# Optimization experiments

Measured on AMD Instinct MI355X. Metric: run time of the kernel, lower is better.

The kernel has to match this reference:

```python
import jax, jax.numpy as jnp
import numpy as np

B, S, D = 2, 2048, 1024
E = 4
H = 4 * D  # MLP hidden; SwiGLU w_v outputs 2*H


def setup_inputs() -> dict:
    key = jax.random.key(0)
    k_x, k_r, k_wv, k_wp = jax.random.split(key, 4)
    x = jax.random.normal(k_x, (B, S, D), dtype=jnp.float32)
    w_router = jax.random.normal(k_r, (D, E), dtype=jnp.float32) * 0.02
    # stacked expert weights, stored [in, out] (transpose of torch Linear)
    w_v = jax.random.normal(k_wv, (E, D, 2 * H), dtype=jnp.float32) * 0.02
    w_proj = jax.random.normal(k_wp, (E, H, D), dtype=jnp.float32) * 0.02
    return {"x": x, "w_router": w_router, "w_v": w_v, "w_proj": w_proj}


def reference(x, w_router, w_v, w_proj):
    # router: softmax then argmax (top-1); output NOT scaled by prob (matches torch src)
    logits = jnp.einsum("bsd,de->bse", x, w_router)
    probs = jax.nn.softmax(logits, axis=-1)
    expert_idx = jnp.argmax(probs, axis=-1)  # [B,S]
    # dense per-expert SwiGLU MLP: gv [E,B,S,2H]
    gv = jnp.einsum("bsd,edh->ebsh", x, w_v)
    gate_raw, value = jnp.split(gv, 2, axis=-1)
    h = gate_raw * jax.nn.sigmoid(gate_raw) * value  # beta=1.0 SiLU gate
    y = jnp.einsum("ebsh,ehd->ebsd", h, w_proj)  # [E,B,S,D]
    onehot = jax.nn.one_hot(expert_idx, w_v.shape[0], dtype=x.dtype)  # [B,S,E]
    return jnp.einsum("bse,ebsd->bsd", onehot, y)
```

## Files before the change

kernel.cpp:

```cpp
#include <hip/hip_runtime.h>


#define TTOK 4096
#define DIN  1024
#define HDIM 4096
#define H2   8192
#define TPAD 4608

typedef float f32x4 __attribute__((ext_vector_type(4)));
typedef __bf16 bf16x8 __attribute__((ext_vector_type(8)));
typedef unsigned short u16x8 __attribute__((ext_vector_type(8)));
typedef unsigned short u16x4 __attribute__((ext_vector_type(4)));

__device__ __forceinline__ unsigned short f2b(float f) {
  unsigned int u = __builtin_bit_cast(unsigned int, f);
  u += 0x7fffu + ((u >> 16) & 1u);
  return (unsigned short)(u >> 16);
}

__device__ __forceinline__ void gload16(const void* g, void* l) {
  __builtin_amdgcn_global_load_lds(
      (const __attribute__((address_space(1))) unsigned int*)g,
      (__attribute__((address_space(3))) unsigned int*)l, 16, 0, 0);
}

__global__ __launch_bounds__(256) void k_router(const float* __restrict__ x,
    const float* __restrict__ wrt, int* __restrict__ eidx,
    int* __restrict__ rank, int* __restrict__ cnt) {
  const int w = threadIdx.x >> 6, lane = threadIdx.x & 63;
  const int t = blockIdx.x * 4 + w;
  const float* xr = x + (size_t)t * DIN;
  const float4* w4 = (const float4*)wrt;
  float a0 = 0.f, a1 = 0.f, a2 = 0.f, a3 = 0.f;
  for (int k = 0; k < DIN; k += 64) {
    float xv = xr[k + lane];
    float4 ww = w4[k + lane];
    a0 += xv * ww.x; a1 += xv * ww.y; a2 += xv * ww.z; a3 += xv * ww.w;
  }
  #pragma unroll
  for (int off = 32; off; off >>= 1) {
    a0 += __shfl_xor(a0, off); a1 += __shfl_xor(a1, off);
    a2 += __shfl_xor(a2, off); a3 += __shfl_xor(a3, off);
  }
  if (lane == 0) {
    int e = 0; float b = a0;
    if (a1 > b) { b = a1; e = 1; }
    if (a2 > b) { b = a2; e = 2; }
    if (a3 > b) { b = a3; e = 3; }
    eidx[t] = e;
    rank[t] = atomicAdd(&cnt[e], 1);
  }
}

__global__ void k_setup(const int* __restrict__ cnt, int* __restrict__ poff,
                        int* __restrict__ tExp, int* __restrict__ tRow,
                        int* __restrict__ nMt) {
  int p = 0, nm = 0;
  for (int e = 0; e < 4; e++) {
    poff[e] = p;
    int mt = (cnt[e] + 127) >> 7;
    for (int i = 0; i < mt; i++) { tExp[nm] = e; tRow[nm] = p + i * 128; nm++; }
    p += mt * 128;
  }
  poff[4] = p;
  *nMt = nm;
}

__global__ __launch_bounds__(256) void k_scatter(const int* __restrict__ eidx,
    const int* __restrict__ rank, const int* __restrict__ poff,
    int* __restrict__ perm) {
  const int t = blockIdx.x * 256 + threadIdx.x;
  const int pos = poff[eidx[t]] + rank[t];
  perm[pos] = t;
}

__global__ __launch_bounds__(256) void k_gather(const float* __restrict__ x,
    const int* __restrict__ perm, unsigned short* __restrict__ A) {
  const int r = blockIdx.x;
  const int t = perm[r];
  unsigned short* dst = A + (size_t)r * DIN + threadIdx.x * 4;
  if (t < 0) {
    u16x4 z{0, 0, 0, 0};
    *(u16x4*)dst = z;
  } else {
    float4 v = *(const float4*)(x + (size_t)t * DIN + threadIdx.x * 4);
    u16x4 o{f2b(v.x), f2b(v.y), f2b(v.z), f2b(v.w)};
    *(u16x4*)dst = o;
  }
}

__global__ __launch_bounds__(256) void k_transpose(const float* __restrict__ src,
    unsigned short* __restrict__ dst, int K, int N) {
  __shared__ __align__(16) unsigned short T[64][72];
  const int n0 = blockIdx.x * 64, k0 = blockIdx.y * 64;
  const size_t eoff = (size_t)blockIdx.z * K * N;
  const int tid = threadIdx.x;
  const int rr = tid >> 4;
  const int cc = (tid & 15) * 4;
  #pragma unroll
  for (int i = 0; i < 4; i++) {
    const int r = rr + i * 16;
    float4 v = *(const float4*)(src + eoff + (size_t)(k0 + r) * N + n0 + cc);
    T[cc + 0][r] = f2b(v.x);
    T[cc + 1][r] = f2b(v.y);
    T[cc + 2][r] = f2b(v.z);
    T[cc + 3][r] = f2b(v.w);
  }
  __syncthreads();
  const int n = tid >> 2, kc = (tid & 3) * 16;
  u16x8 a = *(const u16x8*)&T[n][kc];
  u16x8 b = *(const u16x8*)&T[n][kc + 8];
  unsigned short* dp = dst + eoff + (size_t)(n0 + n) * K + k0 + kc;
  *(u16x8*)(dp) = a;
  *(u16x8*)(dp + 8) = b;
}

__global__ __launch_bounds__(256) void k_gemm1(const unsigned short* __restrict__ A,
    const unsigned short* __restrict__ Wt, unsigned short* __restrict__ Hb,
    const int* __restrict__ tExp, const int* __restrict__ tRow,
    const int* __restrict__ nMt) {
  if ((int)blockIdx.y >= *nMt) return;
  __shared__ __align__(16) unsigned short As[128 * 32];
  __shared__ __align__(16) unsigned short Bg[128 * 32];
  __shared__ __align__(16) unsigned short Bv[128 * 32];
  const int e = tExp[blockIdx.y];
  const int row0 = tRow[blockIdx.y];
  const int n0 = blockIdx.x * 128;
  const int tid = threadIdx.x, lane = tid & 63;
  const int w = tid >> 6, wr = w >> 1, wc = w & 1;
  const int rl = lane >> 2;
  const int kc = (lane & 3) * 8;
  const int mrow = lane & 15, krow = (lane >> 4) * 8;

  const unsigned short* aG  = A  + (size_t)(row0 + w * 16 + rl) * DIN + kc;
  const unsigned short* bgG = Wt + (size_t)e * H2 * DIN
                                 + (size_t)(n0 + w * 16 + rl) * DIN + kc;
  const unsigned short* bvG = bgG + (size_t)HDIM * DIN;

  f32x4 accg[4][4], accv[4][4];
  #pragma unroll
  for (int i = 0; i < 4; i++)
    #pragma unroll
    for (int j = 0; j < 4; j++) {
      accg[i][j] = f32x4{0.f, 0.f, 0.f, 0.f};
      accv[i][j] = f32x4{0.f, 0.f, 0.f, 0.f};
    }

  for (int k0 = 0; k0 < DIN; k0 += 32) {
    gload16(aG + k0,                     &As[w * 512]);
    gload16(aG + k0 + (size_t)64 * DIN,  &As[w * 512 + 2048]);
    gload16(bgG + k0,                    &Bg[w * 512]);
    gload16(bgG + k0 + (size_t)64 * DIN, &Bg[w * 512 + 2048]);
    gload16(bvG + k0,                    &Bv[w * 512]);
    gload16(bvG + k0 + (size_t)64 * DIN, &Bv[w * 512 + 2048]);
    __syncthreads();
    u16x8 af[4], bg[4], bv[4];
    #pragma unroll
    for (int f = 0; f < 4; f++) {
      af[f] = *(const u16x8*)&As[(wr * 64 + f * 16 + mrow) * 32 + krow];
      bg[f] = *(const u16x8*)&Bg[(wc * 64 + f * 16 + mrow) * 32 + krow];
      bv[f] = *(const u16x8*)&Bv[(wc * 64 + f * 16 + mrow) * 32 + krow];
    }
    #pragma unroll
    for (int fn = 0; fn < 4; fn++)
      #pragma unroll
      for (int fm = 0; fm < 4; fm++) {
        accg[fm][fn] = __builtin_amdgcn_mfma_f32_16x16x32_bf16(
            __builtin_bit_cast(bf16x8, af[fm]), __builtin_bit_cast(bf16x8, bg[fn]),
            accg[fm][fn], 0, 0, 0);
        accv[fm][fn] = __builtin_amdgcn_mfma_f32_16x16x32_bf16(
            __builtin_bit_cast(bf16x8, af[fm]), __builtin_bit_cast(bf16x8, bv[fn]),
            accv[fm][fn], 0, 0, 0);
      }
    __syncthreads();
  }
  #pragma unroll
  for (int fm = 0; fm < 4; fm++) {
    const int rbase = row0 + wr * 64 + fm * 16 + (lane >> 4) * 4;
    #pragma unroll
    for (int fn = 0; fn < 4; fn++) {
      const int col = n0 + wc * 64 + fn * 16 + mrow;
      #pragma unroll
      for (int j = 0; j < 4; j++) {
        float g = accg[fm][fn][j];
        float v = accv[fm][fn][j];
        float h = g / (1.f + __expf(-g)) * v;
        Hb[(size_t)(rbase + j) * HDIM + col] = f2b(h);
      }
    }
  }
}

__global__ __launch_bounds__(256) void k_gemm2(const unsigned short* __restrict__ Hb,
    const unsigned short* __restrict__ Wt, float* __restrict__ out,
    const int* __restrict__ tExp, const int* __restrict__ tRow,
    const int* __restrict__ nMt, const int* __restrict__ perm) {
  const int my = blockIdx.y >> 1;
  const int ks = blockIdx.y & 1;
  if (my >= *nMt) return;
  __shared__ __align__(16) unsigned short As[128 * 32];
  __shared__ __align__(16) unsigned short Bs[128 * 32];
  const int e = tExp[my];
  const int row0 = tRow[my];
  const int n0 = blockIdx.x * 128;
  const int tid = threadIdx.x, lane = tid & 63;
  const int w = tid >> 6, wr = w >> 1, wc = w & 1;
  const int rl = lane >> 2, kc = (lane & 3) * 8;
  const int mrow = lane & 15, krow = (lane >> 4) * 8;

  const unsigned short* aG = Hb + (size_t)(row0 + w * 16 + rl) * HDIM + ks * 2048 + kc;
  const unsigned short* bG = Wt + (size_t)e * DIN * HDIM
                                + (size_t)(n0 + w * 16 + rl) * HDIM + ks * 2048 + kc;
  f32x4 acc[4][4];
  #pragma unroll
  for (int i = 0; i < 4; i++)
    #pragma unroll
    for (int j = 0; j < 4; j++) acc[i][j] = f32x4{0.f, 0.f, 0.f, 0.f};

  for (int k0 = 0; k0 < 2048; k0 += 32) {
    gload16(aG + k0,                      &As[w * 512]);
    gload16(aG + k0 + (size_t)64 * HDIM,  &As[w * 512 + 2048]);
    gload16(bG + k0,                      &Bs[w * 512]);
    gload16(bG + k0 + (size_t)64 * HDIM,  &Bs[w * 512 + 2048]);
    __syncthreads();
    u16x8 af[4], bf[4];
    #pragma unroll
    for (int f = 0; f < 4; f++) {
      af[f] = *(const u16x8*)&As[(wr * 64 + f * 16 + mrow) * 32 + krow];
      bf[f] = *(const u16x8*)&Bs[(wc * 64 + f * 16 + mrow) * 32 + krow];
    }
    #pragma unroll
    for (int fn = 0; fn < 4; fn++)
      #pragma unroll
      for (int fm = 0; fm < 4; fm++)
        acc[fm][fn] = __builtin_amdgcn_mfma_f32_16x16x32_bf16(
            __builtin_bit_cast(bf16x8, af[fm]), __builtin_bit_cast(bf16x8, bf[fn]),
            acc[fm][fn], 0, 0, 0);
    __syncthreads();
  }
  #pragma unroll
  for (int fm = 0; fm < 4; fm++) {
    const int rbase = row0 + wr * 64 + fm * 16 + (lane >> 4) * 4;
    #pragma unroll
    for (int fn = 0; fn < 4; fn++) {
      const int col = n0 + wc * 64 + fn * 16 + mrow;
      #pragma unroll
      for (int j = 0; j < 4; j++) {
        const int t = perm[rbase + j];
        if (t >= 0) atomicAdd(&out[(size_t)t * DIN + col], acc[fm][fn][j]);
      }
    }
  }
}

extern "C" void kernel_launch(void* const* d_in, const int* in_sizes, int n_in,
                              void* d_out, int out_size, void* d_ws, size_t ws_size,
                              hipStream_t stream) {
  const float* x        = (const float*)d_in[0];
  const float* w_router = (const float*)d_in[1];
  const float* w_v      = (const float*)d_in[2];
  const float* w_proj   = (const float*)d_in[3];
  float* out = (float*)d_out;
  char* ws = (char*)d_ws;

  int* cnt  = (int*)(ws + 0);
  int* nMt  = (int*)(ws + 16);
  int* poff = (int*)(ws + 32);
  int* tExp = (int*)(ws + 128);
  int* tRow = (int*)(ws + 320);
  int* eidx = (int*)(ws + 512);
  int* rank = (int*)(ws + 512 + 16384);
  int* perm = (int*)(ws + 512 + 32768);
  unsigned short* Abuf = (unsigned short*)(ws + 52224);
  unsigned short* Hbuf = (unsigned short*)(ws + 9489408);
  unsigned short* Wvt  = (unsigned short*)(ws + 47238144);
  unsigned short* Wpt  = (unsigned short*)(ws + 114347008);

  hipMemsetAsync(cnt, 0, 16, stream);
  hipMemsetAsync(perm, 0xFF, TPAD * 4, stream);
  hipMemsetAsync(out, 0, (size_t)out_size * 4, stream);
  k_router<<<TTOK / 4, 256, 0, stream>>>(x, w_router, eidx, rank, cnt);
  k_setup<<<1, 1, 0, stream>>>(cnt, poff, tExp, tRow, nMt);
  k_scatter<<<TTOK / 256, 256, 0, stream>>>(eidx, rank, poff, perm);
  k_gather<<<TPAD, 256, 0, stream>>>(x, perm, Abuf);
  k_transpose<<<dim3(H2 / 64, DIN / 64, 4), 256, 0, stream>>>(w_v, Wvt, DIN, H2);
  k_transpose<<<dim3(DIN / 64, HDIM / 64, 4), 256, 0, stream>>>(w_proj, Wpt, HDIM, DIN);
  k_gemm1<<<dim3(HDIM / 128, 36), 256, 0, stream>>>(Abuf, Wvt, Hbuf, tExp, tRow, nMt);
  k_gemm2<<<dim3(DIN / 128, 72), 256, 0, stream>>>(Hbuf, Wpt, out, tExp, tRow, nMt, perm);
}
```

Baseline: 599.5 us.

## Double-buffer LDS tiles in both expert GEMM kernels

Both grouped GEMM kernels now keep two LDS buffers per operand and issue the async global-to-LDS loads for the next K step before computing the current one. This overlaps global memory latency with the MFMA work and drops one barrier per iteration. In exchange LDS use per block doubles (48KB in gemm1), which may lower occupancy. The single remaining barrier is relied on to make the prefetched data visible, since global_load_lds completion needs a vmcnt wait that the barrier may or may not enforce.

```diff
diff --git a/kernel.cpp b/kernel.cpp
--- a/kernel.cpp
+++ b/kernel.cpp
@@ -120,9 +120,9 @@
     const int* __restrict__ tExp, const int* __restrict__ tRow,
     const int* __restrict__ nMt) {
   if ((int)blockIdx.y >= *nMt) return;
-  __shared__ __align__(16) unsigned short As[128 * 32];
-  __shared__ __align__(16) unsigned short Bg[128 * 32];
-  __shared__ __align__(16) unsigned short Bv[128 * 32];
+  __shared__ __align__(16) unsigned short As[2][128 * 32];
+  __shared__ __align__(16) unsigned short Bg[2][128 * 32];
+  __shared__ __align__(16) unsigned short Bv[2][128 * 32];
   const int e = tExp[blockIdx.y];
   const int row0 = tRow[blockIdx.y];
   const int n0 = blockIdx.x * 128;
@@ -136,6 +136,7 @@
   const unsigned short* bgG = Wt + (size_t)e * H2 * DIN
                                  + (size_t)(n0 + w * 16 + rl) * DIN + kc;
   const unsigned short* bvG = bgG + (size_t)HDIM * DIN;
+  const int ldst = w * 512;
 
   f32x4 accg[4][4], accv[4][4];
   #pragma unroll
@@ -146,20 +147,26 @@
       accv[i][j] = f32x4{0.f, 0.f, 0.f, 0.f};
     }
 
+  auto STAGE = [&](int b, int k0) {
+    gload16(aG + k0,                     &As[b][ldst]);
+    gload16(aG + k0 + (size_t)64 * DIN,  &As[b][ldst + 2048]);
+    gload16(bgG + k0,                    &Bg[b][ldst]);
+    gload16(bgG + k0 + (size_t)64 * DIN, &Bg[b][ldst + 2048]);
+    gload16(bvG + k0,                    &Bv[b][ldst]);
+    gload16(bvG + k0 + (size_t)64 * DIN, &Bv[b][ldst + 2048]);
+  };
+
+  STAGE(0, 0);
+  __syncthreads();
+  int cur = 0;
   for (int k0 = 0; k0 < DIN; k0 += 32) {
-    gload16(aG + k0,                     &As[w * 512]);
-    gload16(aG + k0 + (size_t)64 * DIN,  &As[w * 512 + 2048]);
-    gload16(bgG + k0,                    &Bg[w * 512]);
-    gload16(bgG + k0 + (size_t)64 * DIN, &Bg[w * 512 + 2048]);
-    gload16(bvG + k0,                    &Bv[w * 512]);
-    gload16(bvG + k0 + (size_t)64 * DIN, &Bv[w * 512 + 2048]);
-    __syncthreads();
+    if (k0 + 32 < DIN) STAGE(cur ^ 1, k0 + 32);
     u16x8 af[4], bg[4], bv[4];
     #pragma unroll
     for (int f = 0; f < 4; f++) {
-      af[f] = *(const u16x8*)&As[(wr * 64 + f * 16 + mrow) * 32 + krow];
-      bg[f] = *(const u16x8*)&Bg[(wc * 64 + f * 16 + mrow) * 32 + krow];
-      bv[f] = *(const u16x8*)&Bv[(wc * 64 + f * 16 + mrow) * 32 + krow];
+      af[f] = *(const u16x8*)&As[cur][(wr * 64 + f * 16 + mrow) * 32 + krow];
+      bg[f] = *(const u16x8*)&Bg[cur][(wc * 64 + f * 16 + mrow) * 32 + krow];
+      bv[f] = *(const u16x8*)&Bv[cur][(wc * 64 + f * 16 + mrow) * 32 + krow];
     }
     #pragma unroll
     for (int fn = 0; fn < 4; fn++)
@@ -173,6 +180,7 @@
             accv[fm][fn], 0, 0, 0);
       }
     __syncthreads();
+    cur ^= 1;
   }
   #pragma unroll
   for (int fm = 0; fm < 4; fm++) {
@@ -198,8 +206,8 @@
   const int my = blockIdx.y >> 1;
   const int ks = blockIdx.y & 1;
   if (my >= *nMt) return;
-  __shared__ __align__(16) unsigned short As[128 * 32];
-  __shared__ __align__(16) unsigned short Bs[128 * 32];
+  __shared__ __align__(16) unsigned short As[2][128 * 32];
+  __shared__ __align__(16) unsigned short Bs[2][128 * 32];
   const int e = tExp[my];
   const int row0 = tRow[my];
   const int n0 = blockIdx.x * 128;
@@ -211,23 +219,30 @@
   const unsigned short* aG = Hb + (size_t)(row0 + w * 16 + rl) * HDIM + ks * 2048 + kc;
   const unsigned short* bG = Wt + (size_t)e * DIN * HDIM
                                 + (size_t)(n0 + w * 16 + rl) * HDIM + ks * 2048 + kc;
+  const int ldst = w * 512;
   f32x4 acc[4][4];
   #pragma unroll
   for (int i = 0; i < 4; i++)
     #pragma unroll
     for (int j = 0; j < 4; j++) acc[i][j] = f32x4{0.f, 0.f, 0.f, 0.f};
 
+  auto STAGE = [&](int b, int k0) {
+    gload16(aG + k0,                      &As[b][ldst]);
+    gload16(aG + k0 + (size_t)64 * HDIM,  &As[b][ldst + 2048]);
+    gload16(bG + k0,                      &Bs[b][ldst]);
+    gload16(bG + k0 + (size_t)64 * HDIM,  &Bs[b][ldst + 2048]);
+  };
+
+  STAGE(0, 0);
+  __syncthreads();
+  int cur = 0;
   for (int k0 = 0; k0 < 2048; k0 += 32) {
-    gload16(aG + k0,                      &As[w * 512]);
-    gload16(aG + k0 + (size_t)64 * HDIM,  &As[w * 512 + 2048]);
-    gload16(bG + k0,                      &Bs[w * 512]);
-    gload16(bG + k0 + (size_t)64 * HDIM,  &Bs[w * 512 + 2048]);
-    __syncthreads();
+    if (k0 + 32 < 2048) STAGE(cur ^ 1, k0 + 32);
     u16x8 af[4], bf[4];
     #pragma unroll
     for (int f = 0; f < 4; f++) {
-      af[f] = *(const u16x8*)&As[(wr * 64 + f * 16 + mrow) * 32 + krow];
-      bf[f] = *(const u16x8*)&Bs[(wc * 64 + f * 16 + mrow) * 32 + krow];
+      af[f] = *(const u16x8*)&As[cur][(wr * 64 + f * 16 + mrow) * 32 + krow];
+      bf[f] = *(const u16x8*)&Bs[cur][(wc * 64 + f * 16 + mrow) * 32 + krow];
     }
     #pragma unroll
     for (int fn = 0; fn < 4; fn++)
@@ -237,6 +252,7 @@
             __builtin_bit_cast(bf16x8, af[fm]), __builtin_bit_cast(bf16x8, bf[fn]),
             acc[fm][fn], 0, 0, 0);
     __syncthreads();
+    cur ^= 1;
   }
   #pragma unroll
   for (int fm = 0; fm < 4; fm++) {
```

New measurement: 594.2 us. No clear change (-0.9%).
